# Kernel tuning notes

Hardware: AMD Instinct MI355X
Metric: run time of the kernel (lower is better)

Reference implementation:

```python
import jax, jax.numpy as jnp
import numpy as np

B, S, HID = 16, 1024, 768
H, DH = 12, HID // 12


def setup_inputs() -> dict:
    key = jax.random.key(0)
    ks = jax.random.split(key, 10)
    scale = 1.0 / np.sqrt(HID)
    return {
        "hidden_states": jax.random.normal(ks[0], (B, S, HID), jnp.float32),
        "Wq": jax.random.normal(ks[1], (HID, HID), jnp.float32) * scale,
        "bq": jnp.zeros((HID,), jnp.float32),
        "Wk": jax.random.normal(ks[2], (HID, HID), jnp.float32) * scale,
        "bk": jnp.zeros((HID,), jnp.float32),
        "Wv": jax.random.normal(ks[3], (HID, HID), jnp.float32) * scale,
        "bv": jnp.zeros((HID,), jnp.float32),
        # torch init is zeros; use small randn so the linear-attention correction term is exercised
        "phi_k": jax.random.normal(ks[4], (1, H, DH, 1), jnp.float32) * 0.02,
        "phi_kv": jax.random.normal(ks[5], (1, H, DH, DH), jnp.float32) * 0.02,
    }


def _heads(x):
    # [B,S,HID] -> [B,H,S,DH]
    return x.reshape(B, S, H, DH).transpose(0, 2, 1, 3)


def reference(hidden_states, Wq, bq, Wk, bk, Wv, bv, phi_k, phi_kv):
    q = _heads(hidden_states @ Wq.T + bq)
    k = _heads(hidden_states @ Wk.T + bk)
    v = _heads(hidden_states @ Wv.T + bv)

    # phi(x) = ELU(x / d^0.25) + 1   (dropout disabled: eval-mode reference)
    phi_q = jax.nn.elu(q / jnp.asarray(DH, jnp.float32) ** 0.25) + 1.0

    # full softmax-style attention scores with max-subtract
    A = jnp.einsum("bhsd,bhtd->bhst", q, k) / jnp.sqrt(jnp.asarray(DH, jnp.float32))
    max_A = jnp.max(A, axis=-1, keepdims=True)          # [B,H,S,1]
    exp_max_A = jnp.exp(max_A)
    A = jnp.exp(A - max_A)                              # [B,H,S,S]

    # custom normalizer: softmax mass + linear-attention correction
    D = jnp.sum(A, axis=-1, keepdims=True) + jnp.matmul(phi_q, jnp.abs(phi_k)) / exp_max_A

    ctx = (jnp.matmul(A, v) + jnp.matmul(phi_q, phi_kv) / exp_max_A) / D  # [B,H,S,DH]
    out = ctx.transpose(0, 2, 1, 3).reshape(B, S, HID)
    return out
```

## Files before the change

kernel.cpp:

```cpp
#include <hip/hip_runtime.h>
#include <cstdint>
#include <cstddef>

typedef _Float16 f16x8 __attribute__((ext_vector_type(8)));
typedef _Float16 f16x4 __attribute__((ext_vector_type(4)));
typedef float    f32x4 __attribute__((ext_vector_type(4)));
typedef unsigned u32;
typedef u32      u32x4 __attribute__((ext_vector_type(4)));
typedef const u32 __attribute__((address_space(1)))* gas_ptr;
typedef u32 __attribute__((address_space(3)))* las_ptr;

#define MFMA16(a, b, c) __builtin_amdgcn_mfma_f32_16x16x32_f16((a), (b), (c), 0, 0, 0)

static constexpr int Bb   = 16;
static constexpr int Ss   = 1024;
static constexpr int HID  = 768;
static constexpr int Hh   = 12;
static constexpr int DH   = 64;
static constexpr int Mrows = Bb * Ss;
static constexpr int N3    = 3 * HID;

__global__ void cast_f32_to_f16(const float* __restrict__ x, _Float16* __restrict__ y, int n4) {
    int i = blockIdx.x * 256 + threadIdx.x;
    if (i < n4) {
        float4 v = ((const float4*)x)[i];
        f16x4 o;
        o[0] = (_Float16)v.x; o[1] = (_Float16)v.y;
        o[2] = (_Float16)v.z; o[3] = (_Float16)v.w;
        ((f16x4*)y)[i] = o;
    }
}

__global__ void pack_w(const float* __restrict__ Wq, const float* __restrict__ Wk,
                       const float* __restrict__ Wv, const float* __restrict__ bq,
                       const float* __restrict__ bk, const float* __restrict__ bv,
                       _Float16* __restrict__ Wt, float* __restrict__ bias) {
    int i = blockIdx.x * 256 + threadIdx.x;
    if (i < N3) {
        int wsel = i / HID, j = i - wsel * HID;
        bias[i] = (wsel == 0) ? bq[j] : (wsel == 1) ? bk[j] : bv[j];
    }
    if (i < N3 * HID) {
        int n = i / HID, k = i - n * HID;
        int sel = n / HID;
        int nn  = n - sel * HID;
        const float* W = (sel == 0) ? Wq : (sel == 1) ? Wk : Wv;
        Wt[i] = (_Float16)W[nn * HID + k];
    }
}

__global__ __launch_bounds__(256, 2) void qkv_gemm(
    const _Float16* __restrict__ A, const _Float16* __restrict__ Bt,
    const float* __restrict__ bias,
    _Float16* __restrict__ Qo, _Float16* __restrict__ Ko, _Float16* __restrict__ VTo) {
    __shared__ _Float16 As[128 * 32];
    __shared__ _Float16 Bs[128 * 32];
    const int tid  = threadIdx.x;
    const int lane = tid & 63, wid = tid >> 6;
    const int g = lane >> 4, c = lane & 15;
    const int bm = blockIdx.x & 127, bn = blockIdx.x >> 7;
    const int m0 = bm * 128, n0 = bn * 128;
    const int wm = wid >> 1, wn = wid & 1;

    f32x4 acc[4][4] = {};

    for (int kt = 0; kt < HID; kt += 32) {
        if (kt) __syncthreads();
#pragma unroll
        for (int i = 0; i < 2; ++i) {
            int ch  = i * 256 + wid * 64 + lane;
            int row = ch >> 2;
            int kh  = (ch & 3) << 3;
            __builtin_amdgcn_global_load_lds(
                (gas_ptr)(A + (size_t)(m0 + row) * HID + kt + kh),
                (las_ptr)(As + (i * 256 + wid * 64) * 8), 16, 0, 0);
            __builtin_amdgcn_global_load_lds(
                (gas_ptr)(Bt + (size_t)(n0 + row) * HID + kt + kh),
                (las_ptr)(Bs + (i * 256 + wid * 64) * 8), 16, 0, 0);
        }
        __syncthreads();

        f16x8 af[4], bf[4];
#pragma unroll
        for (int mi = 0; mi < 4; ++mi)
            af[mi] = *(const f16x8*)(As + (wm * 64 + mi * 16 + c) * 32 + g * 8);
#pragma unroll
        for (int ni = 0; ni < 4; ++ni)
            bf[ni] = *(const f16x8*)(Bs + (wn * 64 + ni * 16 + c) * 32 + g * 8);
#pragma unroll
        for (int mi = 0; mi < 4; ++mi)
#pragma unroll
            for (int ni = 0; ni < 4; ++ni)
                acc[mi][ni] = MFMA16(af[mi], bf[ni], acc[mi][ni]);
    }

#pragma unroll
    for (int ni = 0; ni < 4; ++ni) {
        const int col    = n0 + wn * 64 + ni * 16 + c;
        const int which  = col / HID;
        const int within = col - which * HID;
        const int hh = within >> 6, d = within & 63;
        const float bias_v = bias[col];
        const float scl = (which == 0) ? 0.125f : 1.0f;
#pragma unroll
        for (int mi = 0; mi < 4; ++mi) {
            const int rowg0 = m0 + wm * 64 + mi * 16 + g * 4;
            const int bidx = rowg0 >> 10, s0 = rowg0 & 1023;
            const int bh   = bidx * Hh + hh;
            f16x4 hv4;
#pragma unroll
            for (int r = 0; r < 4; ++r)
                hv4[r] = (_Float16)((acc[mi][ni][r] + bias_v) * scl);
            if (which == 2) {
                *(uint2*)(VTo + ((size_t)bh * DH + d) * Ss + s0) = __builtin_bit_cast(uint2, hv4);
            } else if (which == 0) {
#pragma unroll
                for (int r = 0; r < 4; ++r)
                    Qo[((size_t)bh * Ss + s0 + r) * DH + d] = hv4[r];
            } else {
#pragma unroll
                for (int r = 0; r < 4; ++r)
                    Ko[((size_t)bh * Ss + s0 + r) * DH + d] = hv4[r];
            }
        }
    }
}

__global__ __launch_bounds__(256) void attn_kernel(
    const _Float16* __restrict__ Q, const _Float16* __restrict__ K,
    const _Float16* __restrict__ VT, const float* __restrict__ phi_k,
    const float* __restrict__ phi_kv, float* __restrict__ out) {
    __shared__ _Float16 Kb[2][64 * 64];
    __shared__ _Float16 Vb[2][64 * 64];

    const int tid  = threadIdx.x;
    const int lane = tid & 63, w = tid >> 6;
    const int g = lane >> 4, c = lane & 15;

    const int wg = (blockIdx.x & 7) * 192 + (blockIdx.x >> 3);
    const int bh = wg >> 3, qt = wg & 7;
    const int b = bh / Hh, h = bh - b * Hh;
    const size_t base = (size_t)bh * Ss * DH;
    const _Float16* Kg = K + base;
    const _Float16* Vg = VT + base;

    const int srow = lane >> 3;
    const int scol = (((lane & 7) ^ srow) << 4) >> 1;
    const int sw = (c & 7) << 4;

    const _Float16* Qp = Q + base + (size_t)(qt * 128 + w * 32 + c) * DH + g * 8;
    f16x8 aq[2][2];
    aq[0][0] = *(const f16x8*)(Qp);
    aq[0][1] = *(const f16x8*)(Qp + 32);
    aq[1][0] = *(const f16x8*)(Qp + 16 * DH);
    aq[1][1] = *(const f16x8*)(Qp + 16 * DH + 32);

    float part[2] = {0.f, 0.f};
    f32x4 acco[2][4] = {};

    auto stage = [&](int bf, int t0) {
#pragma unroll
        for (int i = 0; i < 2; ++i) {
            const int row0 = w * 16 + i * 8;
            __builtin_amdgcn_global_load_lds(
                (gas_ptr)(Kg + (size_t)(t0 + row0 + srow) * DH + scol),
                (las_ptr)(&Kb[bf][row0 * 64]), 16, 0, 0);
            __builtin_amdgcn_global_load_lds(
                (gas_ptr)(Vg + (size_t)(row0 + srow) * Ss + t0 + scol),
                (las_ptr)(&Vb[bf][row0 * 64]), 16, 0, 0);
        }
    };

    stage(0, 0);
    __syncthreads();

    for (int t0 = 0; t0 < Ss; t0 += 64) {
        const int bf = (t0 >> 6) & 1;
        if (t0 + 64 < Ss) stage(bf ^ 1, t0 + 64);

        f32x4 z[2][4];
#pragma unroll
        for (int nt = 0; nt < 4; ++nt) {
            const char* kb = (const char*)&Kb[bf][0] + (nt * 16 + c) * 128;
            f16x8 bk0 = *(const f16x8*)(kb + ((g * 16) ^ sw));
            f16x8 bk1 = *(const f16x8*)(kb + ((64 + g * 16) ^ sw));
            f32x4 z0 = {}, z1 = {};
            z0 = MFMA16(bk0, aq[0][0], z0);
            z0 = MFMA16(bk1, aq[0][1], z0);
            z1 = MFMA16(bk0, aq[1][0], z1);
            z1 = MFMA16(bk1, aq[1][1], z1);
            z[0][nt] = z0;
            z[1][nt] = z1;
        }

        f16x8 pb[2][2];
#pragma unroll
        for (int mb = 0; mb < 2; ++mb) {
#pragma unroll
            for (int kk = 0; kk < 2; ++kk) {
                float e0 = __expf(z[mb][2 * kk][0]);
                float e1 = __expf(z[mb][2 * kk][1]);
                float e2 = __expf(z[mb][2 * kk][2]);
                float e3 = __expf(z[mb][2 * kk][3]);
                float e4 = __expf(z[mb][2 * kk + 1][0]);
                float e5 = __expf(z[mb][2 * kk + 1][1]);
                float e6 = __expf(z[mb][2 * kk + 1][2]);
                float e7 = __expf(z[mb][2 * kk + 1][3]);
                part[mb] += (e0 + e1 + e2 + e3) + (e4 + e5 + e6 + e7);
                u32x4 pk;
                pk[0] = __builtin_bit_cast(u32, __builtin_amdgcn_cvt_pkrtz(e0, e1));
                pk[1] = __builtin_bit_cast(u32, __builtin_amdgcn_cvt_pkrtz(e2, e3));
                pk[2] = __builtin_bit_cast(u32, __builtin_amdgcn_cvt_pkrtz(e4, e5));
                pk[3] = __builtin_bit_cast(u32, __builtin_amdgcn_cvt_pkrtz(e6, e7));
                pb[mb][kk] = __builtin_bit_cast(f16x8, pk);
            }
        }

#pragma unroll
        for (int nd = 0; nd < 4; ++nd) {
            const char* vb = (const char*)&Vb[bf][0] + (nd * 16 + c) * 128;
#pragma unroll
            for (int kk = 0; kk < 2; ++kk) {
                f16x4 vlo = *(const f16x4*)(vb + ((kk * 64 + 8 * g) ^ sw));
                f16x4 vhi = *(const f16x4*)(vb + ((kk * 64 + 32 + 8 * g) ^ sw));
                f16x8 va = __builtin_shufflevector(vlo, vhi, 0, 1, 2, 3, 4, 5, 6, 7);
                acco[0][nd] = MFMA16(va, pb[0][kk], acco[0][nd]);
                acco[1][nd] = MFMA16(va, pb[1][kk], acco[1][nd]);
            }
        }
        __syncthreads();
    }

    const float* phk = phi_k + h * DH;
    const float* pkv = phi_kv + h * DH * DH;

    f16x8 pq2[2][2];
    float invD[2];
#pragma unroll
    for (int mb = 0; mb < 2; ++mb) {
        const _Float16* Qr = Q + base + (size_t)(qt * 128 + w * 32 + mb * 16 + c) * DH;
        float dot = 0.f;
#pragma unroll
        for (int kk = 0; kk < 2; ++kk) {
            f16x4 qa = *(const f16x4*)(Qr + kk * 32 + 4 * g);
            f16x4 qb = *(const f16x4*)(Qr + kk * 32 + 16 + 4 * g);
            float4 fka = *(const float4*)(phk + kk * 32 + 4 * g);
            float4 fkb = *(const float4*)(phk + kk * 32 + 16 + 4 * g);
            const float fa[4] = {fka.x, fka.y, fka.z, fka.w};
            const float fb[4] = {fkb.x, fkb.y, fkb.z, fkb.w};
            f16x8 pq;
#pragma unroll
            for (int j = 0; j < 4; ++j) {
                float x0 = (float)qa[j] * 2.82842712f;
                float x1 = (float)qb[j] * 2.82842712f;
                float p0 = (x0 > 0.f) ? (x0 + 1.f) : __expf(x0);
                float p1 = (x1 > 0.f) ? (x1 + 1.f) : __expf(x1);
                dot += p0 * fabsf(fa[j]) + p1 * fabsf(fb[j]);
                pq[j]     = (_Float16)p0;
                pq[4 + j] = (_Float16)p1;
            }
            pq2[mb][kk] = pq;
        }
        dot += __shfl_xor(dot, 16);
        dot += __shfl_xor(dot, 32);
        float s = part[mb];
        s += __shfl_xor(s, 16);
        s += __shfl_xor(s, 32);
        invD[mb] = 1.f / (s + dot);
    }

#pragma unroll
    for (int nd = 0; nd < 4; ++nd) {
        f16x8 fa[2];
#pragma unroll
        for (int kk = 0; kk < 2; ++kk) {
            f16x8 t;
#pragma unroll
            for (int j = 0; j < 8; ++j) {
                int dh = kk * 32 + 16 * (j >> 2) + 4 * g + (j & 3);
                t[j] = (_Float16)pkv[dh * DH + nd * 16 + c];
            }
            fa[kk] = t;
        }
#pragma unroll
        for (int mb = 0; mb < 2; ++mb) {
            f32x4 cc = {};
            cc = MFMA16(fa[0], pq2[mb][0], cc);
            cc = MFMA16(fa[1], pq2[mb][1], cc);
            f32x4 o = (acco[mb][nd] + cc) * invD[mb];
            const int srow_o = qt * 128 + w * 32 + mb * 16 + c;
            float* op = out + ((size_t)b * Ss + srow_o) * HID + h * DH + nd * 16 + 4 * g;
            *(f32x4*)op = o;
        }
    }
}

extern "C" void kernel_launch(void* const* d_in, const int* in_sizes, int n_in,
                              void* d_out, int out_size, void* d_ws, size_t ws_size,
                              hipStream_t stream) {
    (void)in_sizes; (void)n_in; (void)out_size;
    const float* hs   = (const float*)d_in[0];
    const float* Wq   = (const float*)d_in[1];
    const float* bq   = (const float*)d_in[2];
    const float* Wk   = (const float*)d_in[3];
    const float* bk   = (const float*)d_in[4];
    const float* Wv   = (const float*)d_in[5];
    const float* bv   = (const float*)d_in[6];
    const float* phik = (const float*)d_in[7];
    const float* phikv= (const float*)d_in[8];
    float* out = (float*)d_out;

    char* ws = (char*)d_ws;
    constexpr size_t szA   = (size_t)Mrows * HID * 2;
    constexpr size_t szWt  = (size_t)N3 * HID * 2;
    constexpr size_t szBia = (size_t)N3 * 4;
    constexpr size_t szQ   = (size_t)Bb * Hh * Ss * DH * 2;
    _Float16* A16  = (_Float16*)(ws);
    _Float16* Wt   = (_Float16*)(ws + szA);
    float*    bias = (float*)(ws + szA + szWt);
    _Float16* Qb   = (_Float16*)(ws + szA + szWt + szBia);
    _Float16* Kb   = (_Float16*)(ws + szA + szWt + szBia + szQ);
    _Float16* VTb  = (_Float16*)(ws + szA + szWt + szBia + 2 * szQ);
    (void)ws_size;

    cast_f32_to_f16<<<(Mrows * HID / 4 + 255) / 256, 256, 0, stream>>>(hs, A16, Mrows * HID / 4);
    pack_w<<<(N3 * HID + 255) / 256, 256, 0, stream>>>(Wq, Wk, Wv, bq, bk, bv, Wt, bias);
    qkv_gemm<<<dim3((Mrows / 128) * (N3 / 128)), 256, 0, stream>>>(A16, Wt, bias, Qb, Kb, VTb);
    attn_kernel<<<dim3(Bb * Hh * (Ss / 128)), 256, 0, stream>>>(Qb, Kb, VTb, phik, phikv, out);
}
```

Before: 204.0 us.

## Fuse fp32-to-fp16 cast into QKV GEMM with register-prefetched swizzled LDS tiles

Removes the separate cast kernel: the GEMM now reads fp32 hidden states directly, converts them in registers and writes fp16 into XOR-swizzled LDS. K-tile grows to 64 and the next tile's global loads are issued before the current tile's MFMAs, giving register-staged double buffering. The Q scale folds in log2(e) so the attention kernel can use a raw exp2, and the phi scale is adjusted to match. V is stored in a permuted sequence order so the attention kernel reads one 16-byte vector instead of two 8-byte loads. The cost is doubled A-tile global traffic in fp32 across the 18 column blocks and higher register pressure.

```diff
diff --git a/kernel.cpp b/kernel.cpp
--- a/kernel.cpp
+++ b/kernel.cpp
@@ -6,7 +6,6 @@
 typedef _Float16 f16x4 __attribute__((ext_vector_type(4)));
 typedef float    f32x4 __attribute__((ext_vector_type(4)));
 typedef unsigned u32;
-typedef u32      u32x4 __attribute__((ext_vector_type(4)));
 typedef const u32 __attribute__((address_space(1)))* gas_ptr;
 typedef u32 __attribute__((address_space(3)))* las_ptr;
 
@@ -20,16 +19,8 @@
 static constexpr int Mrows = Bb * Ss;
 static constexpr int N3    = 3 * HID;
 
-__global__ void cast_f32_to_f16(const float* __restrict__ x, _Float16* __restrict__ y, int n4) {
-    int i = blockIdx.x * 256 + threadIdx.x;
-    if (i < n4) {
-        float4 v = ((const float4*)x)[i];
-        f16x4 o;
-        o[0] = (_Float16)v.x; o[1] = (_Float16)v.y;
-        o[2] = (_Float16)v.z; o[3] = (_Float16)v.w;
-        ((f16x4*)y)[i] = o;
-    }
-}
+static constexpr float QSCL  = 0.125f * 1.44269504088896f;
+static constexpr float PHSCL = 1.9605161f;
 
 __global__ void pack_w(const float* __restrict__ Wq, const float* __restrict__ Wk,
                        const float* __restrict__ Wv, const float* __restrict__ bq,
@@ -49,49 +40,95 @@
     }
 }
 
-__global__ __launch_bounds__(256, 2) void qkv_gemm(
-    const _Float16* __restrict__ A, const _Float16* __restrict__ Bt,
+__global__ __launch_bounds__(256) void qkv_gemm(
+    const float* __restrict__ A, const _Float16* __restrict__ Bt,
     const float* __restrict__ bias,
     _Float16* __restrict__ Qo, _Float16* __restrict__ Ko, _Float16* __restrict__ VTo) {
-    __shared__ _Float16 As[128 * 32];
-    __shared__ _Float16 Bs[128 * 32];
+    __shared__ _Float16 As[128 * 64];
+    __shared__ _Float16 Bs[128 * 64];
     const int tid  = threadIdx.x;
-    const int lane = tid & 63, wid = tid >> 6;
+    const int lane = tid & 63;
     const int g = lane >> 4, c = lane & 15;
     const int bm = blockIdx.x & 127, bn = blockIdx.x >> 7;
     const int m0 = bm * 128, n0 = bn * 128;
+    const int wid = tid >> 6;
     const int wm = wid >> 1, wn = wid & 1;
 
     f32x4 acc[4][4] = {};
-
-    for (int kt = 0; kt < HID; kt += 32) {
-        if (kt) __syncthreads();
-#pragma unroll
-        for (int i = 0; i < 2; ++i) {
-            int ch  = i * 256 + wid * 64 + lane;
-            int row = ch >> 2;
-            int kh  = (ch & 3) << 3;
-            __builtin_amdgcn_global_load_lds(
-                (gas_ptr)(A + (size_t)(m0 + row) * HID + kt + kh),
-                (las_ptr)(As + (i * 256 + wid * 64) * 8), 16, 0, 0);
-            __builtin_amdgcn_global_load_lds(
-                (gas_ptr)(Bt + (size_t)(n0 + row) * HID + kt + kh),
-                (las_ptr)(Bs + (i * 256 + wid * 64) * 8), 16, 0, 0);
-        }
+    float4 a0[4], a1[4];
+    uint4  bst[4];
+
+    int srow[4], sc8[4], soff[4];
+#pragma unroll
+    for (int i = 0; i < 4; ++i) {
+        int ch = i * 256 + tid;
+        srow[i] = ch >> 3;
+        sc8[i]  = ch & 7;
+        soff[i] = srow[i] * 128 + ((sc8[i] ^ (srow[i] & 7)) << 4);
+    }
+
+    auto issue_loads = [&](int kt) {
+#pragma unroll
+        for (int i = 0; i < 4; ++i) {
+            const float* ap = A + (size_t)(m0 + srow[i]) * HID + kt + sc8[i] * 8;
+            a0[i] = *(const float4*)ap;
+            a1[i] = *(const float4*)(ap + 4);
+            bst[i] = *(const uint4*)(Bt + (size_t)(n0 + srow[i]) * HID + kt + sc8[i] * 8);
+        }
+    };
+    auto write_lds = [&]() {
+#pragma unroll
+        for (int i = 0; i < 4; ++i) {
+            uint4 av;
+            av.x = __builtin_bit_cast(u32, __builtin_amdgcn_cvt_pkrtz(a0[i].x, a0[i].y));
+            av.y = __builtin_bit_cast(u32, __builtin_amdgcn_cvt_pkrtz(a0[i].z, a0[i].w));
+            av.z = __builtin_bit_cast(u32, __builtin_amdgcn_cvt_pkrtz(a1[i].x, a1[i].y));
+            av.w = __builtin_bit_cast(u32, __builtin_amdgcn_cvt_pkrtz(a1[i].z, a1[i].w));
+            *(uint4*)((char*)As + soff[i]) = av;
+            *(uint4*)((char*)Bs + soff[i]) = bst[i];
+        }
+    };
+
+    issue_loads(0);
+    write_lds();
+    __syncthreads();
+
+    for (int kt = 0; kt < HID; kt += 64) {
+        const bool more = (kt + 64) < HID;
+        if (more) issue_loads(kt + 64);
+
+        f16x8 af[4][2], bf[4][2];
+#pragma unroll
+        for (int mi = 0; mi < 4; ++mi) {
+            const int row = wm * 64 + mi * 16 + c;
+            const char* rp = (const char*)As + row * 128;
+            const int k7 = row & 7;
+#pragma unroll
+            for (int kk = 0; kk < 2; ++kk)
+                af[mi][kk] = *(const f16x8*)(rp + (((kk * 4 + g) ^ k7) << 4));
+        }
+#pragma unroll
+        for (int ni = 0; ni < 4; ++ni) {
+            const int row = wn * 64 + ni * 16 + c;
+            const char* rp = (const char*)Bs + row * 128;
+            const int k7 = row & 7;
+#pragma unroll
+            for (int kk = 0; kk < 2; ++kk)
+                bf[ni][kk] = *(const f16x8*)(rp + (((kk * 4 + g) ^ k7) << 4));
+        }
+#pragma unroll
+        for (int kk = 0; kk < 2; ++kk)
+#pragma unroll
+            for (int mi = 0; mi < 4; ++mi)
+#pragma unroll
+                for (int ni = 0; ni < 4; ++ni)
+                    acc[mi][ni] = MFMA16(af[mi][kk], bf[ni][kk], acc[mi][ni]);
+
         __syncthreads();
-
-        f16x8 af[4], bf[4];
-#pragma unroll
-        for (int mi = 0; mi < 4; ++mi)
-            af[mi] = *(const f16x8*)(As + (wm * 64 + mi * 16 + c) * 32 + g * 8);
-#pragma unroll
-        for (int ni = 0; ni < 4; ++ni)
-            bf[ni] = *(const f16x8*)(Bs + (wn * 64 + ni * 16 + c) * 32 + g * 8);
-#pragma unroll
-        for (int mi = 0; mi < 4; ++mi)
-#pragma unroll
-            for (int ni = 0; ni < 4; ++ni)
-                acc[mi][ni] = MFMA16(af[mi], bf[ni], acc[mi][ni]);
+        if (more) {
+            write_lds();
+            __syncthreads();
+        }
     }
 
 #pragma unroll
@@ -101,7 +138,7 @@
         const int within = col - which * HID;
         const int hh = within >> 6, d = within & 63;
         const float bias_v = bias[col];
-        const float scl = (which == 0) ? 0.125f : 1.0f;
+        const float scl = (which == 0) ? QSCL : 1.0f;
 #pragma unroll
         for (int mi = 0; mi < 4; ++mi) {
             const int rowg0 = m0 + wm * 64 + mi * 16 + g * 4;
@@ -112,7 +149,9 @@
             for (int r = 0; r < 4; ++r)
                 hv4[r] = (_Float16)((acc[mi][ni][r] + bias_v) * scl);
             if (which == 2) {
-                *(uint2*)(VTo + ((size_t)bh * DH + d) * Ss + s0) = __builtin_bit_cast(uint2, hv4);
+                const int base64 = (m0 + wm * 64) & 1023;
+                const int p = 32 * (mi >> 1) + 8 * g + 4 * (mi & 1);
+                *(uint2*)(VTo + ((size_t)bh * DH + d) * Ss + base64 + p) = __builtin_bit_cast(uint2, hv4);
             } else if (which == 0) {
 #pragma unroll
                 for (int r = 0; r < 4; ++r)
@@ -198,20 +237,20 @@
         for (int mb = 0; mb < 2; ++mb) {
 #pragma unroll
             for (int kk = 0; kk < 2; ++kk) {
-                float e0 = __expf(z[mb][2 * kk][0]);
-                float e1 = __expf(z[mb][2 * kk][1]);
-                float e2 = __expf(z[mb][2 * kk][2]);
-                float e3 = __expf(z[mb][2 * kk][3]);
-                float e4 = __expf(z[mb][2 * kk + 1][0]);
-                float e5 = __expf(z[mb][2 * kk + 1][1]);
-                float e6 = __expf(z[mb][2 * kk + 1][2]);
-                float e7 = __expf(z[mb][2 * kk + 1][3]);
+                float e0 = __builtin_amdgcn_exp2f(z[mb][2 * kk][0]);
+                float e1 = __builtin_amdgcn_exp2f(z[mb][2 * kk][1]);
+                float e2 = __builtin_amdgcn_exp2f(z[mb][2 * kk][2]);
+                float e3 = __builtin_amdgcn_exp2f(z[mb][2 * kk][3]);
+                float e4 = __builtin_amdgcn_exp2f(z[mb][2 * kk + 1][0]);
+                float e5 = __builtin_amdgcn_exp2f(z[mb][2 * kk + 1][1]);
+                float e6 = __builtin_amdgcn_exp2f(z[mb][2 * kk + 1][2]);
+                float e7 = __builtin_amdgcn_exp2f(z[mb][2 * kk + 1][3]);
                 part[mb] += (e0 + e1 + e2 + e3) + (e4 + e5 + e6 + e7);
-                u32x4 pk;
-                pk[0] = __builtin_bit_cast(u32, __builtin_amdgcn_cvt_pkrtz(e0, e1));
-                pk[1] = __builtin_bit_cast(u32, __builtin_amdgcn_cvt_pkrtz(e2, e3));
-                pk[2] = __builtin_bit_cast(u32, __builtin_amdgcn_cvt_pkrtz(e4, e5));
-                pk[3] = __builtin_bit_cast(u32, __builtin_amdgcn_cvt_pkrtz(e6, e7));
+                uint4 pk;
+                pk.x = __builtin_bit_cast(u32, __builtin_amdgcn_cvt_pkrtz(e0, e1));
+                pk.y = __builtin_bit_cast(u32, __builtin_amdgcn_cvt_pkrtz(e2, e3));
+                pk.z = __builtin_bit_cast(u32, __builtin_amdgcn_cvt_pkrtz(e4, e5));
+                pk.w = __builtin_bit_cast(u32, __builtin_amdgcn_cvt_pkrtz(e6, e7));
                 pb[mb][kk] = __builtin_bit_cast(f16x8, pk);
             }
         }
@@ -221,9 +260,7 @@
             const char* vb = (const char*)&Vb[bf][0] + (nd * 16 + c) * 128;
 #pragma unroll
             for (int kk = 0; kk < 2; ++kk) {
-                f16x4 vlo = *(const f16x4*)(vb + ((kk * 64 + 8 * g) ^ sw));
-                f16x4 vhi = *(const f16x4*)(vb + ((kk * 64 + 32 + 8 * g) ^ sw));
-                f16x8 va = __builtin_shufflevector(vlo, vhi, 0, 1, 2, 3, 4, 5, 6, 7);
+                f16x8 va = *(const f16x8*)(vb + ((kk * 64 + g * 16) ^ sw));
                 acco[0][nd] = MFMA16(va, pb[0][kk], acco[0][nd]);
                 acco[1][nd] = MFMA16(va, pb[1][kk], acco[1][nd]);
             }
@@ -251,8 +288,8 @@
             f16x8 pq;
 #pragma unroll
             for (int j = 0; j < 4; ++j) {
-                float x0 = (float)qa[j] * 2.82842712f;
-                float x1 = (float)qb[j] * 2.82842712f;
+                float x0 = (float)qa[j] * PHSCL;
+                float x1 = (float)qb[j] * PHSCL;
                 float p0 = (x0 > 0.f) ? (x0 + 1.f) : __expf(x0);
                 float p1 = (x1 > 0.f) ? (x1 + 1.f) : __expf(x1);
                 dot += p0 * fabsf(fa[j]) + p1 * fabsf(fb[j]);
@@ -311,20 +348,17 @@
     float* out = (float*)d_out;
 
     char* ws = (char*)d_ws;
-    constexpr size_t szA   = (size_t)Mrows * HID * 2;
     constexpr size_t szWt  = (size_t)N3 * HID * 2;
     constexpr size_t szBia = (size_t)N3 * 4;
     constexpr size_t szQ   = (size_t)Bb * Hh * Ss * DH * 2;
-    _Float16* A16  = (_Float16*)(ws);
-    _Float16* Wt   = (_Float16*)(ws + szA);
-    float*    bias = (float*)(ws + szA + szWt);
-    _Float16* Qb   = (_Float16*)(ws + szA + szWt + szBia);
-    _Float16* Kb   = (_Float16*)(ws + szA + szWt + szBia + szQ);
-    _Float16* VTb  = (_Float16*)(ws + szA + szWt + szBia + 2 * szQ);
+    _Float16* Wt   = (_Float16*)(ws);
+    float*    bias = (float*)(ws + szWt);
+    _Float16* Qb   = (_Float16*)(ws + szWt + szBia);
+    _Float16* Kb   = (_Float16*)(ws + szWt + szBia + szQ);
+    _Float16* VTb  = (_Float16*)(ws + szWt + szBia + 2 * szQ);
     (void)ws_size;
 
-    cast_f32_to_f16<<<(Mrows * HID / 4 + 255) / 256, 256, 0, stream>>>(hs, A16, Mrows * HID / 4);
     pack_w<<<(N3 * HID + 255) / 256, 256, 0, stream>>>(Wq, Wk, Wv, bq, bk, bv, Wt, bias);
-    qkv_gemm<<<dim3((Mrows / 128) * (N3 / 128)), 256, 0, stream>>>(A16, Wt, bias, Qb, Kb, VTb);
+    qkv_gemm<<<dim3((Mrows / 128) * (N3 / 128)), 256, 0, stream>>>(hs, Wt, bias, Qb, Kb, VTb);
     attn_kernel<<<dim3(Bb * Hh * (Ss / 128)), 256, 0, stream>>>(Qb, Kb, VTb, phik, phikv, out);
 }
```

After: 316.4 us. 1.55x slower.

## Swizzle GEMM LDS tiles, permute V^T columns for wide loads, use exp2

Applied to the files above, without the earlier changes.

Applies an XOR swizzle to the projection GEMM's LDS A/B tiles to reduce bank conflicts on fragment reads. It also reorders the sequence positions written into V^T so the attention kernel can fetch each V fragment with one 16-byte LDS load instead of two 8-byte loads plus a shuffle. In addition, log2(e) is folded into the Q scale so softmax uses native exp2, and the phi scale constant is adjusted to match. The V^T permutation must stay consistent with the P fragment ordering, and the folded scale changes the meaning of the stored Q.

```diff
diff --git a/kernel.cpp b/kernel.cpp
--- a/kernel.cpp
+++ b/kernel.cpp
@@ -6,7 +6,6 @@
 typedef _Float16 f16x4 __attribute__((ext_vector_type(4)));
 typedef float    f32x4 __attribute__((ext_vector_type(4)));
 typedef unsigned u32;
-typedef u32      u32x4 __attribute__((ext_vector_type(4)));
 typedef const u32 __attribute__((address_space(1)))* gas_ptr;
 typedef u32 __attribute__((address_space(3)))* las_ptr;
 
@@ -19,6 +18,9 @@
 static constexpr int DH   = 64;
 static constexpr int Mrows = Bb * Ss;
 static constexpr int N3    = 3 * HID;
+
+static constexpr float QSCL  = 0.125f * 1.44269504088896f;
+static constexpr float PHSCL = 1.9605161f;
 
 __global__ void cast_f32_to_f16(const float* __restrict__ x, _Float16* __restrict__ y, int n4) {
     int i = blockIdx.x * 256 + threadIdx.x;
@@ -70,7 +72,7 @@
         for (int i = 0; i < 2; ++i) {
             int ch  = i * 256 + wid * 64 + lane;
             int row = ch >> 2;
-            int kh  = (ch & 3) << 3;
+            int kh  = ((ch & 3) ^ ((row >> 1) & 3)) << 3;
             __builtin_amdgcn_global_load_lds(
                 (gas_ptr)(A + (size_t)(m0 + row) * HID + kt + kh),
                 (las_ptr)(As + (i * 256 + wid * 64) * 8), 16, 0, 0);
@@ -82,11 +84,15 @@
 
         f16x8 af[4], bf[4];
 #pragma unroll
-        for (int mi = 0; mi < 4; ++mi)
-            af[mi] = *(const f16x8*)(As + (wm * 64 + mi * 16 + c) * 32 + g * 8);
-#pragma unroll
-        for (int ni = 0; ni < 4; ++ni)
-            bf[ni] = *(const f16x8*)(Bs + (wn * 64 + ni * 16 + c) * 32 + g * 8);
+        for (int mi = 0; mi < 4; ++mi) {
+            const int row = wm * 64 + mi * 16 + c;
+            af[mi] = *(const f16x8*)((const char*)As + row * 64 + ((g ^ ((row >> 1) & 3)) << 4));
+        }
+#pragma unroll
+        for (int ni = 0; ni < 4; ++ni) {
+            const int row = wn * 64 + ni * 16 + c;
+            bf[ni] = *(const f16x8*)((const char*)Bs + row * 64 + ((g ^ ((row >> 1) & 3)) << 4));
+        }
 #pragma unroll
         for (int mi = 0; mi < 4; ++mi)
 #pragma unroll
@@ -101,7 +107,7 @@
         const int within = col - which * HID;
         const int hh = within >> 6, d = within & 63;
         const float bias_v = bias[col];
-        const float scl = (which == 0) ? 0.125f : 1.0f;
+        const float scl = (which == 0) ? QSCL : 1.0f;
 #pragma unroll
         for (int mi = 0; mi < 4; ++mi) {
             const int rowg0 = m0 + wm * 64 + mi * 16 + g * 4;
@@ -112,7 +118,9 @@
             for (int r = 0; r < 4; ++r)
                 hv4[r] = (_Float16)((acc[mi][ni][r] + bias_v) * scl);
             if (which == 2) {
-                *(uint2*)(VTo + ((size_t)bh * DH + d) * Ss + s0) = __builtin_bit_cast(uint2, hv4);
+                const int base64 = (m0 + wm * 64) & 1023;
+                const int p = 32 * (mi >> 1) + 8 * g + 4 * (mi & 1);
+                *(uint2*)(VTo + ((size_t)bh * DH + d) * Ss + base64 + p) = __builtin_bit_cast(uint2, hv4);
             } else if (which == 0) {
 #pragma unroll
                 for (int r = 0; r < 4; ++r)
@@ -198,20 +206,20 @@
         for (int mb = 0; mb < 2; ++mb) {
 #pragma unroll
             for (int kk = 0; kk < 2; ++kk) {
-                float e0 = __expf(z[mb][2 * kk][0]);
-                float e1 = __expf(z[mb][2 * kk][1]);
-                float e2 = __expf(z[mb][2 * kk][2]);
-                float e3 = __expf(z[mb][2 * kk][3]);
-                float e4 = __expf(z[mb][2 * kk + 1][0]);
-                float e5 = __expf(z[mb][2 * kk + 1][1]);
-                float e6 = __expf(z[mb][2 * kk + 1][2]);
-                float e7 = __expf(z[mb][2 * kk + 1][3]);
+                float e0 = __builtin_amdgcn_exp2f(z[mb][2 * kk][0]);
+                float e1 = __builtin_amdgcn_exp2f(z[mb][2 * kk][1]);
+                float e2 = __builtin_amdgcn_exp2f(z[mb][2 * kk][2]);
+                float e3 = __builtin_amdgcn_exp2f(z[mb][2 * kk][3]);
+                float e4 = __builtin_amdgcn_exp2f(z[mb][2 * kk + 1][0]);
+                float e5 = __builtin_amdgcn_exp2f(z[mb][2 * kk + 1][1]);
+                float e6 = __builtin_amdgcn_exp2f(z[mb][2 * kk + 1][2]);
+                float e7 = __builtin_amdgcn_exp2f(z[mb][2 * kk + 1][3]);
                 part[mb] += (e0 + e1 + e2 + e3) + (e4 + e5 + e6 + e7);
-                u32x4 pk;
-                pk[0] = __builtin_bit_cast(u32, __builtin_amdgcn_cvt_pkrtz(e0, e1));
-                pk[1] = __builtin_bit_cast(u32, __builtin_amdgcn_cvt_pkrtz(e2, e3));
-                pk[2] = __builtin_bit_cast(u32, __builtin_amdgcn_cvt_pkrtz(e4, e5));
-                pk[3] = __builtin_bit_cast(u32, __builtin_amdgcn_cvt_pkrtz(e6, e7));
+                uint4 pk;
+                pk.x = __builtin_bit_cast(u32, __builtin_amdgcn_cvt_pkrtz(e0, e1));
+                pk.y = __builtin_bit_cast(u32, __builtin_amdgcn_cvt_pkrtz(e2, e3));
+                pk.z = __builtin_bit_cast(u32, __builtin_amdgcn_cvt_pkrtz(e4, e5));
+                pk.w = __builtin_bit_cast(u32, __builtin_amdgcn_cvt_pkrtz(e6, e7));
                 pb[mb][kk] = __builtin_bit_cast(f16x8, pk);
             }
         }
@@ -221,9 +229,7 @@
             const char* vb = (const char*)&Vb[bf][0] + (nd * 16 + c) * 128;
 #pragma unroll
             for (int kk = 0; kk < 2; ++kk) {
-                f16x4 vlo = *(const f16x4*)(vb + ((kk * 64 + 8 * g) ^ sw));
-                f16x4 vhi = *(const f16x4*)(vb + ((kk * 64 + 32 + 8 * g) ^ sw));
-                f16x8 va = __builtin_shufflevector(vlo, vhi, 0, 1, 2, 3, 4, 5, 6, 7);
+                f16x8 va = *(const f16x8*)(vb + ((kk * 64 + g * 16) ^ sw));
                 acco[0][nd] = MFMA16(va, pb[0][kk], acco[0][nd]);
                 acco[1][nd] = MFMA16(va, pb[1][kk], acco[1][nd]);
             }
@@ -251,8 +257,8 @@
             f16x8 pq;
 #pragma unroll
             for (int j = 0; j < 4; ++j) {
-                float x0 = (float)qa[j] * 2.82842712f;
-                float x1 = (float)qb[j] * 2.82842712f;
+                float x0 = (float)qa[j] * PHSCL;
+                float x1 = (float)qb[j] * PHSCL;
                 float p0 = (x0 > 0.f) ? (x0 + 1.f) : __expf(x0);
                 float p1 = (x1 > 0.f) ? (x1 + 1.f) : __expf(x1);
                 dot += p0 * fabsf(fa[j]) + p1 * fabsf(fb[j]);
```

Result: faster. 182.9 us (-10.3%).
